# Performance work log

Hardware: AMD Instinct MI355X
Metric: run time of the kernel (lower is better)

## Reference

```python
import jax, jax.numpy as jnp
import numpy as np

B, S, D = 2, 2048, 1024
H, KS = 16, 64

def setup_inputs() -> dict:
    key = jax.random.key(0)
    k1, k2, k3, k4, k5 = jax.random.split(key, 5)
    return {
        "x": jax.random.normal(k1, (B, S, D), dtype=jnp.float32),
        "Wq": jax.random.normal(k2, (D, KS, H), dtype=jnp.float32) * 0.02,
        "Wk": jax.random.normal(k3, (D, KS, H), dtype=jnp.float32) * 0.02,
        "Wv": jax.random.normal(k4, (D, KS, H), dtype=jnp.float32) * 0.02,
        "kernel": jax.random.normal(k5, (H * KS, KS), dtype=jnp.float32) * 0.02,
    }

def reference(x, Wq, Wk, Wv, kernel):
    b, s, d = x.shape
    ks, h = Wq.shape[1], Wq.shape[2]
    # projections: heads-last layout [b, s, ks, h]
    q = jnp.einsum('bsd,dkh->bskh', x, Wq)
    k = jnp.einsum('bsd,dkh->bskh', x, Wk)
    v = jnp.einsum('bsd,dkh->bskh', x, Wv)
    # scores [b, i(query), l(key), h]
    scores = jnp.einsum('bikh,blkh->bilh', q, k) / jnp.sqrt(jnp.float32(ks))
    # strictly-upper-triangular (future) mask, as in the original:
    # band_part(ones,0,-1) - eye  ->  1 where l > i
    li = jnp.arange(s)
    mask = (li[None, :] > li[:, None]).astype(jnp.float32)  # [s, s]
    scores = scores - 1e8 * mask[None, :, :, None]
    weights = jax.nn.softmax(scores, axis=2)  # softmax over key axis l
    heads = jnp.einsum('bilh,blkh->bikh', weights, v)  # [b, s, ks, h]
    heads = heads.reshape(b, s, ks * h)  # row-major flatten of (ks, h), matching tf.reshape
    return heads @ kernel  # [b, s, ks]
```

## Files before the change

kernel.cpp:

```cpp
#include <hip/hip_runtime.h>
#include <hip/hip_bf16.h>

#define BB 2
#define SS 2048
#define DD 1024
#define HH 16
#define KSZ 64

typedef __attribute__((ext_vector_type(8))) short s16x8;
typedef __attribute__((ext_vector_type(4))) float f32x4;
typedef __attribute__((ext_vector_type(8))) unsigned short u16x8;
typedef __attribute__((ext_vector_type(4))) unsigned short u16x4;
typedef __attribute__((ext_vector_type(2))) unsigned int u32x2;
typedef unsigned short u16;

__device__ __forceinline__ u16 bf16rne(float f) {
  unsigned int u = __float_as_uint(f);
  unsigned int r = (u + 0x7FFFu + ((u >> 16) & 1u)) >> 16;
  return (u16)r;
}

__device__ __forceinline__ void lds_dma16(const u16* g, u16* l) {
  __builtin_amdgcn_global_load_lds(
      (const __attribute__((address_space(1))) unsigned int*)(const void*)g,
      (__attribute__((address_space(3))) unsigned int*)(void*)l, 16, 0, 0);
}

__global__ __launch_bounds__(256) void prep_all(
    const float* __restrict__ x, const float* __restrict__ Wq,
    const float* __restrict__ Wk, const float* __restrict__ Wv,
    const float* __restrict__ kern, u16* __restrict__ xb,
    u16* __restrict__ Wt, u16* __restrict__ BpT) {
  __shared__ float Ts[64][65];
  const int bid = blockIdx.x;
  const int tid = threadIdx.x;
  if (bid < 2048) {
    int idx = (bid * 256 + tid) * 8;
    float4 a = *(const float4*)(x + idx);
    float4 b = *(const float4*)(x + idx + 4);
    u16x8 v;
    v[0] = bf16rne(a.x); v[1] = bf16rne(a.y); v[2] = bf16rne(a.z); v[3] = bf16rne(a.w);
    v[4] = bf16rne(b.x); v[5] = bf16rne(b.y); v[6] = bf16rne(b.z); v[7] = bf16rne(b.w);
    *(u16x8*)(xb + idx) = v;
  } else if (bid < 2816) {
    const int bx = bid - 2048;
    const int p = bx >> 8, rem = bx & 255;
    const int d0 = (rem & 15) * 64, n0 = (rem >> 4) * 64;
    const float* W = (p == 0) ? Wq : (p == 1) ? Wk : Wv;
    u16* Wo = Wt + (size_t)p * DD * DD;
    #pragma unroll
    for (int i = 0; i < 4; ++i) {
      int f4 = tid + i * 256;
      int r = f4 >> 4, c4 = f4 & 15;
      float4 v = *(const float4*)(W + (size_t)(d0 + r) * DD + n0 + c4 * 4);
      Ts[r][c4 * 4 + 0] = v.x; Ts[r][c4 * 4 + 1] = v.y;
      Ts[r][c4 * 4 + 2] = v.z; Ts[r][c4 * 4 + 3] = v.w;
    }
    __syncthreads();
    #pragma unroll
    for (int i = 0; i < 4; ++i) {
      int ch = tid + i * 256;
      int n = ch >> 4, d4 = ch & 15;
      u16x4 o;
      #pragma unroll
      for (int j = 0; j < 4; ++j) o[j] = bf16rne(Ts[d4 * 4 + j][n]);
      *(u16x4*)(Wo + (size_t)(n0 + n) * DD + d0 + d4 * 4) = o;
    }
  } else {
    const int n = bid - 2816;
    const int k4 = tid * 4;
    u16x4 o;
    #pragma unroll
    for (int j = 0; j < 4; ++j) {
      int kp = k4 + j;
      int h = kp >> 6, k = kp & 63;
      o[j] = bf16rne(kern[(size_t)(k * HH + h) * KSZ + n]);
    }
    *(u16x4*)(BpT + (size_t)n * (HH * KSZ) + k4) = o;
  }
}

__global__ __launch_bounds__(256) void proj_kernel(
    const u16* __restrict__ xb, const u16* __restrict__ Wt,
    u16* __restrict__ qkvT) {
  const int xcd = blockIdx.x & 7;
  const int idx = blockIdx.x >> 3;
  const int mt = (xcd >> 1) * 8 + (idx & 7);
  const int nt = (xcd & 1) * 4 + ((idx >> 3) & 3);
  const int p  = idx >> 5;
  const int m0 = mt * 128, n0 = nt * 128;
  const u16* W = Wt + (size_t)p * DD * DD;
  u16* outp = qkvT + (size_t)p * (BB * HH * SS * KSZ);

  __shared__ __align__(16) unsigned char raw[34816];
  u16* As0 = (u16*)raw;
  u16* Bs0 = As0 + 128 * 32;
  u16* As1 = Bs0 + 128 * 32;
  u16* Bs1 = As1 + 128 * 32;
  u16* Cs  = (u16*)raw;

  const int tid = threadIdx.x;
  const int wave = tid >> 6, lane = tid & 63;
  const int g = lane >> 4, c = lane & 15;
  const int mbase = (wave & 1) * 64, nbase = (wave >> 1) * 64;

  const int lr = lane >> 2, lc = lane & 3;
  const int swz = (lc ^ ((lr >> 1) & 3)) * 8;
  const int rA0 = (wave * 2 + 0) * 16;
  const int rA1 = (wave * 2 + 1) * 16;
  const u16* srcA0 = xb + (size_t)(m0 + rA0 + lr) * DD + swz;
  const u16* srcA1 = xb + (size_t)(m0 + rA1 + lr) * DD + swz;
  const u16* srcB0 = W  + (size_t)(n0 + rA0 + lr) * DD + swz;
  const u16* srcB1 = W  + (size_t)(n0 + rA1 + lr) * DD + swz;
  const int sl0 = rA0 * 32, sl1 = rA1 * 32;

  f32x4 acc[4][4];
  #pragma unroll
  for (int i = 0; i < 4; ++i)
    #pragma unroll
    for (int j = 0; j < 4; ++j) acc[i][j] = {0.f, 0.f, 0.f, 0.f};

  lds_dma16(srcA0, As0 + sl0);  lds_dma16(srcA1, As0 + sl1);
  lds_dma16(srcB0, Bs0 + sl0);  lds_dma16(srcB1, Bs0 + sl1);
  __syncthreads();

  const int jsw = (c >> 1) & 3;
  #pragma unroll 2
  for (int t = 0; t < 32; ++t) {
    u16* Ac = (t & 1) ? As1 : As0;
    u16* Bc = (t & 1) ? Bs1 : Bs0;
    if (t < 31) {
      u16* An = (t & 1) ? As0 : As1;
      u16* Bn = (t & 1) ? Bs0 : Bs1;
      const int ko = (t + 1) * 32;
      lds_dma16(srcA0 + ko, An + sl0);  lds_dma16(srcA1 + ko, An + sl1);
      lds_dma16(srcB0 + ko, Bn + sl0);  lds_dma16(srcB1 + ko, Bn + sl1);
    }
    s16x8 af[4], bfr[4];
    #pragma unroll
    for (int mf = 0; mf < 4; ++mf)
      af[mf] = *(const s16x8*)&Ac[(mbase + mf * 16 + c) * 32 + ((g ^ jsw) * 8)];
    #pragma unroll
    for (int nf = 0; nf < 4; ++nf)
      bfr[nf] = *(const s16x8*)&Bc[(nbase + nf * 16 + c) * 32 + ((g ^ jsw) * 8)];
    #pragma unroll
    for (int mf = 0; mf < 4; ++mf)
      #pragma unroll
      for (int nf = 0; nf < 4; ++nf)
        acc[mf][nf] = __builtin_amdgcn_mfma_f32_16x16x32_bf16(
            af[mf], bfr[nf], acc[mf][nf], 0, 0, 0);
    __syncthreads();
  }

  const float cscale = (p == 0) ? 0.125f * 1.44269504f : 1.0f;
  #pragma unroll
  for (int mf = 0; mf < 4; ++mf)
    #pragma unroll
    for (int nf = 0; nf < 4; ++nf)
      #pragma unroll
      for (int r = 0; r < 4; ++r)
        Cs[(mbase + mf * 16 + g * 4 + r) * 136 + nbase + nf * 16 + c] =
            bf16rne(acc[mf][nf][r] * cscale);
  __syncthreads();
  const int b = m0 >> 11;
  if (p < 2) {
    int hh = tid >> 4, si = tid & 15;
    #pragma unroll
    for (int i = 0; i < 8; ++i) {
      int row = i * 16 + si;
      int s = (m0 + row) & 2047;
      u16x8 v;
      #pragma unroll
      for (int kp = 0; kp < 8; ++kp) v[kp] = Cs[row * 136 + kp * 16 + hh];
      *(u16x8*)(outp + ((size_t)(b * HH + hh) * SS + s) * KSZ + (n0 >> 4)) = v;
    }
  } else {
    const int s0 = m0 & 2047;
    #pragma unroll
    for (int i = 0; i < 8; ++i) {
      int chunk = tid + i * 256;
      int colid = chunk >> 4;
      int hh = colid >> 3, kp = colid & 7;
      int s8 = chunk & 15;
      u16x8 v;
      #pragma unroll
      for (int j = 0; j < 8; ++j) v[j] = Cs[(s8 * 8 + j) * 136 + kp * 16 + hh];
      *(u16x8*)(outp + ((size_t)(b * HH + hh) * KSZ + (n0 >> 4) + kp) * SS +
                s0 + s8 * 8) = v;
    }
  }
}

__global__ __launch_bounds__(256) void attn_kernel(
    const u16* __restrict__ qkvT, u16* __restrict__ headsB) {
  const int bid = blockIdx.x;
  const int hb = bid & 31;
  const int u  = bid >> 5;
  const int it = (u & 1) ? (31 - (u >> 1)) : (u >> 1);
  const int h = hb & 15, b = hb >> 4;
  const size_t plane = (size_t)(b * HH + h) * SS * KSZ;
  const size_t PSZ = (size_t)BB * HH * SS * KSZ;
  const u16* Qg = qkvT + plane;
  const u16* Kg = qkvT + PSZ + plane;
  const u16* Vg = qkvT + 2 * PSZ + plane;

  __shared__ u16 Ks[2][64 * 64];
  __shared__ u16 Vt[2][64 * 64];
  __shared__ u16 Ps[64 * 72];

  const int tid = threadIdx.x;
  const int lane = tid & 63;
  const int g = lane >> 4, c = lane & 15;
  const int wq0 = (tid >> 6) * 16;
  const int sr = tid >> 3, sc = tid & 7;
  const int soA = sr * 64 + ((sc ^ (sr & 7)) * 8);
  const int soB = soA + 32 * 64;

  s16x8 bq0 = *(const s16x8*)(Qg + (size_t)(it * 64 + wq0 + c) * KSZ + g * 8);
  s16x8 bq1 = *(const s16x8*)(Qg + (size_t)(it * 64 + wq0 + c) * KSZ + 32 + g * 8);

  u16x8 kr0 = *(const u16x8*)(Kg + (size_t)sr * KSZ + sc * 8);
  u16x8 kr1 = *(const u16x8*)(Kg + (size_t)(sr + 32) * KSZ + sc * 8);
  u16x8 vr0 = *(const u16x8*)(Vg + (size_t)sr * SS + sc * 8);
  u16x8 vr1 = *(const u16x8*)(Vg + (size_t)(sr + 32) * SS + sc * 8);
  *(u16x8*)&Ks[0][soA] = kr0; *(u16x8*)&Ks[0][soB] = kr1;
  *(u16x8*)&Vt[0][soA] = vr0; *(u16x8*)&Vt[0][soB] = vr1;
  if (it >= 1) {
    kr0 = *(const u16x8*)(Kg + (size_t)(64 + sr) * KSZ + sc * 8);
    kr1 = *(const u16x8*)(Kg + (size_t)(64 + sr + 32) * KSZ + sc * 8);
    vr0 = *(const u16x8*)(Vg + (size_t)sr * SS + 64 + sc * 8);
    vr1 = *(const u16x8*)(Vg + (size_t)(sr + 32) * SS + 64 + sc * 8);
  }
  __syncthreads();

  f32x4 o[4];
  #pragma unroll
  for (int mf = 0; mf < 4; ++mf) o[mf] = {0.f, 0.f, 0.f, 0.f};
  float l_i = 0.f;
  const int cswz = c & 7;

  #pragma unroll 1
  for (int t = 0; t <= it; ++t) {
    const int buf = t & 1;
    if (t < it) {
      const int nb = buf ^ 1;
      *(u16x8*)&Ks[nb][soA] = kr0; *(u16x8*)&Ks[nb][soB] = kr1;
      *(u16x8*)&Vt[nb][soA] = vr0; *(u16x8*)&Vt[nb][soB] = vr1;
      if (t + 2 <= it) {
        const int kv2 = t + 2;
        kr0 = *(const u16x8*)(Kg + (size_t)(kv2 * 64 + sr) * KSZ + sc * 8);
        kr1 = *(const u16x8*)(Kg + (size_t)(kv2 * 64 + sr + 32) * KSZ + sc * 8);
        vr0 = *(const u16x8*)(Vg + (size_t)sr * SS + kv2 * 64 + sc * 8);
        vr1 = *(const u16x8*)(Vg + (size_t)(sr + 32) * SS + kv2 * 64 + sc * 8);
      }
    }
    f32x4 s[4];
    #pragma unroll
    for (int mf = 0; mf < 4; ++mf) s[mf] = {0.f, 0.f, 0.f, 0.f};
    #pragma unroll
    for (int ks = 0; ks < 2; ++ks) {
      const s16x8 bq = ks ? bq1 : bq0;
      #pragma unroll
      for (int mf = 0; mf < 4; ++mf) {
        s16x8 ak = *(const s16x8*)&Ks[buf][(mf * 16 + c) * 64 +
                                          (((ks * 4 + g) ^ cswz) * 8)];
        s[mf] = __builtin_amdgcn_mfma_f32_16x16x32_bf16(ak, bq, s[mf], 0, 0, 0);
      }
    }
    if (t == it) {
      const int qloc = wq0 + c;
      #pragma unroll
      for (int mf = 0; mf < 4; ++mf)
        #pragma unroll
        for (int r = 0; r < 4; ++r)
          if (mf * 16 + g * 4 + r > qloc) s[mf][r] = -1e30f;
    }
    float ps = 0.f;
    #pragma unroll
    for (int mf = 0; mf < 4; ++mf) {
      float p0 = __builtin_amdgcn_exp2f(s[mf][0]);
      float p1 = __builtin_amdgcn_exp2f(s[mf][1]);
      float p2 = __builtin_amdgcn_exp2f(s[mf][2]);
      float p3 = __builtin_amdgcn_exp2f(s[mf][3]);
      ps += (p0 + p1) + (p2 + p3);
      u32x2 d;
      d[0] = (__float_as_uint(p0) >> 16) | (__float_as_uint(p1) & 0xFFFF0000u);
      d[1] = (__float_as_uint(p2) >> 16) | (__float_as_uint(p3) & 0xFFFF0000u);
      *(u32x2*)&Ps[(wq0 + c) * 72 + mf * 16 + g * 4] = d;
    }
    l_i += ps;
    #pragma unroll
    for (int ks = 0; ks < 2; ++ks) {
      s16x8 bp = *(const s16x8*)&Ps[(wq0 + c) * 72 + ks * 32 + g * 8];
      #pragma unroll
      for (int mf = 0; mf < 4; ++mf) {
        s16x8 av = *(const s16x8*)&Vt[buf][(mf * 16 + c) * 64 +
                                           (((ks * 4 + g) ^ cswz) * 8)];
        o[mf] = __builtin_amdgcn_mfma_f32_16x16x32_bf16(av, bp, o[mf], 0, 0, 0);
      }
    }
    __syncthreads();
  }
  l_i += __shfl_xor(l_i, 16);
  l_i += __shfl_xor(l_i, 32);
  const float inv = 1.0f / l_i;
  const int q = it * 64 + wq0 + c;
  #pragma unroll
  for (int mf = 0; mf < 4; ++mf) {
    u16x4 hv;
    #pragma unroll
    for (int r = 0; r < 4; ++r) hv[r] = bf16rne(o[mf][r] * inv);
    *(u16x4*)(headsB + plane + (size_t)q * KSZ + mf * 16 + g * 4) = hv;
  }
}

__global__ __launch_bounds__(256) void out_kernel(
    const u16* __restrict__ headsB, const u16* __restrict__ BpT,
    float* __restrict__ out) {
  const int m0 = blockIdx.x * 16;
  const int tid = threadIdx.x;
  const int wave = tid >> 6, lane = tid & 63;
  const int g = lane >> 4, c = lane & 15;

  const int m = m0 + c;
  const int b = m >> 11, s = m & 2047;

  f32x4 acc[4];
  #pragma unroll
  for (int nf = 0; nf < 4; ++nf) acc[nf] = {0.f, 0.f, 0.f, 0.f};

  #pragma unroll
  for (int it = 0; it < 8; ++it) {
    const int kb = wave * 256 + it * 32;
    const int hh = kb >> 6, kk = (kb & 63) + g * 8;
    s16x8 a = *(const s16x8*)(headsB +
        ((size_t)(b * HH + hh) * SS + s) * KSZ + kk);
    #pragma unroll
    for (int nf = 0; nf < 4; ++nf) {
      s16x8 bf = *(const s16x8*)(BpT +
          (size_t)(nf * 16 + c) * (HH * KSZ) + kb + g * 8);
      acc[nf] = __builtin_amdgcn_mfma_f32_16x16x32_bf16(a, bf, acc[nf], 0, 0, 0);
    }
  }

  __shared__ __align__(16) float red[4][64][16];
  #pragma unroll
  for (int nf = 0; nf < 4; ++nf)
    *(f32x4*)&red[wave][lane][nf * 4] = acc[nf];
  __syncthreads();

  const int mi = tid >> 4, n4 = (tid & 15) * 4;
  const int gg = mi >> 2, rr = mi & 3;
  float4 res;
  float* rp = &res.x;
  #pragma unroll
  for (int j = 0; j < 4; ++j) {
    int n = n4 + j;
    int cc = n & 15, nf = n >> 4;
    rp[j] = red[0][gg * 16 + cc][nf * 4 + rr] + red[1][gg * 16 + cc][nf * 4 + rr] +
            red[2][gg * 16 + cc][nf * 4 + rr] + red[3][gg * 16 + cc][nf * 4 + rr];
  }
  *(float4*)(out + (size_t)(m0 + mi) * KSZ + n4) = res;
}

extern "C" void kernel_launch(void* const* d_in, const int* in_sizes, int n_in,
                              void* d_out, int out_size, void* d_ws, size_t ws_size,
                              hipStream_t stream) {
  const float* x    = (const float*)d_in[0];
  const float* Wq   = (const float*)d_in[1];
  const float* Wk   = (const float*)d_in[2];
  const float* Wv   = (const float*)d_in[3];
  const float* kern = (const float*)d_in[4];
  float* out = (float*)d_out;

  u16* xb     = (u16*)d_ws;
  u16* Wt     = xb + (size_t)4096 * 1024;
  u16* qkvT   = Wt + (size_t)3 * 1024 * 1024;
  u16* headsB = qkvT + (size_t)3 * BB * HH * SS * KSZ;
  u16* BpT    = headsB + (size_t)BB * HH * SS * KSZ;

  prep_all<<<dim3(2880), 256, 0, stream>>>(x, Wq, Wk, Wv, kern, xb, Wt, BpT);
  proj_kernel<<<dim3(768), 256, 0, stream>>>(xb, Wt, qkvT);
  attn_kernel<<<dim3(1024), 256, 0, stream>>>(qkvT, headsB);
  out_kernel<<<dim3(256), 256, 0, stream>>>(headsB, BpT, out);
}
```

Baseline: 160.8 us.

## Halve projection M tile and load V fragments directly from global in attention

The projection GEMM moves from 128x128 to 64x128 tiles with twice as many blocks, a smaller LDS footprint and a launch bound of 6 waves-per-EU, aiming for better occupancy and CU fill. The attention kernel no longer stages V through shared memory. Each wave loads its V MFMA operands straight from global memory every KV step, which removes the LDS stores and reads for V. In exchange, the four waves now fetch the same V data redundantly, and those loads are not prefetched across iterations, so latency may be exposed.

```diff
diff --git a/kernel.cpp b/kernel.cpp
--- a/kernel.cpp
+++ b/kernel.cpp
@@ -80,48 +80,48 @@
   }
 }
 
-__global__ __launch_bounds__(256) void proj_kernel(
+__global__ __launch_bounds__(256, 6) void proj_kernel(
     const u16* __restrict__ xb, const u16* __restrict__ Wt,
     u16* __restrict__ qkvT) {
   const int xcd = blockIdx.x & 7;
   const int idx = blockIdx.x >> 3;
-  const int mt = (xcd >> 1) * 8 + (idx & 7);
-  const int nt = (xcd & 1) * 4 + ((idx >> 3) & 3);
-  const int p  = idx >> 5;
-  const int m0 = mt * 128, n0 = nt * 128;
+  const int mt = (xcd >> 1) * 16 + (idx & 15);
+  const int nt = (xcd & 1) * 4 + ((idx >> 4) & 3);
+  const int p  = idx >> 6;
+  const int m0 = mt * 64, n0 = nt * 128;
   const u16* W = Wt + (size_t)p * DD * DD;
   u16* outp = qkvT + (size_t)p * (BB * HH * SS * KSZ);
 
-  __shared__ __align__(16) unsigned char raw[34816];
+  __shared__ __align__(16) unsigned char raw[24576];
   u16* As0 = (u16*)raw;
-  u16* Bs0 = As0 + 128 * 32;
+  u16* Bs0 = As0 + 64 * 32;
   u16* As1 = Bs0 + 128 * 32;
-  u16* Bs1 = As1 + 128 * 32;
+  u16* Bs1 = As1 + 64 * 32;
   u16* Cs  = (u16*)raw;
 
   const int tid = threadIdx.x;
   const int wave = tid >> 6, lane = tid & 63;
   const int g = lane >> 4, c = lane & 15;
-  const int mbase = (wave & 1) * 64, nbase = (wave >> 1) * 64;
+  const int mbase = (wave & 1) * 32, nbase = (wave >> 1) * 64;
 
   const int lr = lane >> 2, lc = lane & 3;
   const int swz = (lc ^ ((lr >> 1) & 3)) * 8;
-  const int rA0 = (wave * 2 + 0) * 16;
-  const int rA1 = (wave * 2 + 1) * 16;
-  const u16* srcA0 = xb + (size_t)(m0 + rA0 + lr) * DD + swz;
-  const u16* srcA1 = xb + (size_t)(m0 + rA1 + lr) * DD + swz;
-  const u16* srcB0 = W  + (size_t)(n0 + rA0 + lr) * DD + swz;
-  const u16* srcB1 = W  + (size_t)(n0 + rA1 + lr) * DD + swz;
-  const int sl0 = rA0 * 32, sl1 = rA1 * 32;
-
-  f32x4 acc[4][4];
-  #pragma unroll
-  for (int i = 0; i < 4; ++i)
+  const int rA  = wave * 16;
+  const int rB0 = (wave * 2 + 0) * 16;
+  const int rB1 = (wave * 2 + 1) * 16;
+  const u16* srcA  = xb + (size_t)(m0 + rA  + lr) * DD + swz;
+  const u16* srcB0 = W  + (size_t)(n0 + rB0 + lr) * DD + swz;
+  const u16* srcB1 = W  + (size_t)(n0 + rB1 + lr) * DD + swz;
+  const int slA = rA * 32, slB0 = rB0 * 32, slB1 = rB1 * 32;
+
+  f32x4 acc[2][4];
+  #pragma unroll
+  for (int i = 0; i < 2; ++i)
     #pragma unroll
     for (int j = 0; j < 4; ++j) acc[i][j] = {0.f, 0.f, 0.f, 0.f};
 
-  lds_dma16(srcA0, As0 + sl0);  lds_dma16(srcA1, As0 + sl1);
-  lds_dma16(srcB0, Bs0 + sl0);  lds_dma16(srcB1, Bs0 + sl1);
+  lds_dma16(srcA, As0 + slA);
+  lds_dma16(srcB0, Bs0 + slB0);  lds_dma16(srcB1, Bs0 + slB1);
   __syncthreads();
 
   const int jsw = (c >> 1) & 3;
@@ -133,18 +133,18 @@
       u16* An = (t & 1) ? As0 : As1;
       u16* Bn = (t & 1) ? Bs0 : Bs1;
       const int ko = (t + 1) * 32;
-      lds_dma16(srcA0 + ko, An + sl0);  lds_dma16(srcA1 + ko, An + sl1);
-      lds_dma16(srcB0 + ko, Bn + sl0);  lds_dma16(srcB1 + ko, Bn + sl1);
-    }
-    s16x8 af[4], bfr[4];
-    #pragma unroll
-    for (int mf = 0; mf < 4; ++mf)
+      lds_dma16(srcA + ko, An + slA);
+      lds_dma16(srcB0 + ko, Bn + slB0);  lds_dma16(srcB1 + ko, Bn + slB1);
+    }
+    s16x8 af[2], bfr[4];
+    #pragma unroll
+    for (int mf = 0; mf < 2; ++mf)
       af[mf] = *(const s16x8*)&Ac[(mbase + mf * 16 + c) * 32 + ((g ^ jsw) * 8)];
     #pragma unroll
     for (int nf = 0; nf < 4; ++nf)
       bfr[nf] = *(const s16x8*)&Bc[(nbase + nf * 16 + c) * 32 + ((g ^ jsw) * 8)];
     #pragma unroll
-    for (int mf = 0; mf < 4; ++mf)
+    for (int mf = 0; mf < 2; ++mf)
       #pragma unroll
       for (int nf = 0; nf < 4; ++nf)
         acc[mf][nf] = __builtin_amdgcn_mfma_f32_16x16x32_bf16(
@@ -154,7 +154,7 @@
 
   const float cscale = (p == 0) ? 0.125f * 1.44269504f : 1.0f;
   #pragma unroll
-  for (int mf = 0; mf < 4; ++mf)
+  for (int mf = 0; mf < 2; ++mf)
     #pragma unroll
     for (int nf = 0; nf < 4; ++nf)
       #pragma unroll
@@ -166,7 +166,7 @@
   if (p < 2) {
     int hh = tid >> 4, si = tid & 15;
     #pragma unroll
-    for (int i = 0; i < 8; ++i) {
+    for (int i = 0; i < 4; ++i) {
       int row = i * 16 + si;
       int s = (m0 + row) & 2047;
       u16x8 v;
@@ -177,11 +177,11 @@
   } else {
     const int s0 = m0 & 2047;
     #pragma unroll
-    for (int i = 0; i < 8; ++i) {
+    for (int i = 0; i < 4; ++i) {
       int chunk = tid + i * 256;
-      int colid = chunk >> 4;
+      int colid = chunk >> 3;
       int hh = colid >> 3, kp = colid & 7;
-      int s8 = chunk & 15;
+      int s8 = chunk & 7;
       u16x8 v;
       #pragma unroll
       for (int j = 0; j < 8; ++j) v[j] = Cs[(s8 * 8 + j) * 136 + kp * 16 + hh];
@@ -205,7 +205,6 @@
   const u16* Vg = qkvT + 2 * PSZ + plane;
 
   __shared__ u16 Ks[2][64 * 64];
-  __shared__ u16 Vt[2][64 * 64];
   __shared__ u16 Ps[64 * 72];
 
   const int tid = threadIdx.x;
@@ -219,17 +218,14 @@
   s16x8 bq0 = *(const s16x8*)(Qg + (size_t)(it * 64 + wq0 + c) * KSZ + g * 8);
   s16x8 bq1 = *(const s16x8*)(Qg + (size_t)(it * 64 + wq0 + c) * KSZ + 32 + g * 8);
 
+  const u16* vb = Vg + (size_t)c * SS + g * 8;
+
   u16x8 kr0 = *(const u16x8*)(Kg + (size_t)sr * KSZ + sc * 8);
   u16x8 kr1 = *(const u16x8*)(Kg + (size_t)(sr + 32) * KSZ + sc * 8);
-  u16x8 vr0 = *(const u16x8*)(Vg + (size_t)sr * SS + sc * 8);
-  u16x8 vr1 = *(const u16x8*)(Vg + (size_t)(sr + 32) * SS + sc * 8);
   *(u16x8*)&Ks[0][soA] = kr0; *(u16x8*)&Ks[0][soB] = kr1;
-  *(u16x8*)&Vt[0][soA] = vr0; *(u16x8*)&Vt[0][soB] = vr1;
   if (it >= 1) {
     kr0 = *(const u16x8*)(Kg + (size_t)(64 + sr) * KSZ + sc * 8);
     kr1 = *(const u16x8*)(Kg + (size_t)(64 + sr + 32) * KSZ + sc * 8);
-    vr0 = *(const u16x8*)(Vg + (size_t)sr * SS + 64 + sc * 8);
-    vr1 = *(const u16x8*)(Vg + (size_t)(sr + 32) * SS + 64 + sc * 8);
   }
   __syncthreads();
 
@@ -245,15 +241,19 @@
     if (t < it) {
       const int nb = buf ^ 1;
       *(u16x8*)&Ks[nb][soA] = kr0; *(u16x8*)&Ks[nb][soB] = kr1;
-      *(u16x8*)&Vt[nb][soA] = vr0; *(u16x8*)&Vt[nb][soB] = vr1;
       if (t + 2 <= it) {
         const int kv2 = t + 2;
         kr0 = *(const u16x8*)(Kg + (size_t)(kv2 * 64 + sr) * KSZ + sc * 8);
         kr1 = *(const u16x8*)(Kg + (size_t)(kv2 * 64 + sr + 32) * KSZ + sc * 8);
-        vr0 = *(const u16x8*)(Vg + (size_t)sr * SS + kv2 * 64 + sc * 8);
-        vr1 = *(const u16x8*)(Vg + (size_t)(sr + 32) * SS + kv2 * 64 + sc * 8);
       }
     }
+    s16x8 av[2][4];
+    #pragma unroll
+    for (int ks = 0; ks < 2; ++ks)
+      #pragma unroll
+      for (int mf = 0; mf < 4; ++mf)
+        av[ks][mf] = *(const s16x8*)(vb + (size_t)(mf * 16) * SS +
+                                     t * 64 + ks * 32);
     f32x4 s[4];
     #pragma unroll
     for (int mf = 0; mf < 4; ++mf) s[mf] = {0.f, 0.f, 0.f, 0.f};
@@ -293,11 +293,9 @@
     for (int ks = 0; ks < 2; ++ks) {
       s16x8 bp = *(const s16x8*)&Ps[(wq0 + c) * 72 + ks * 32 + g * 8];
       #pragma unroll
-      for (int mf = 0; mf < 4; ++mf) {
-        s16x8 av = *(const s16x8*)&Vt[buf][(mf * 16 + c) * 64 +
-                                           (((ks * 4 + g) ^ cswz) * 8)];
-        o[mf] = __builtin_amdgcn_mfma_f32_16x16x32_bf16(av, bp, o[mf], 0, 0, 0);
-      }
+      for (int mf = 0; mf < 4; ++mf)
+        o[mf] = __builtin_amdgcn_mfma_f32_16x16x32_bf16(av[ks][mf], bp, o[mf],
+                                                        0, 0, 0);
     }
     __syncthreads();
   }
@@ -380,7 +378,7 @@
   u16* BpT    = headsB + (size_t)BB * HH * SS * KSZ;
 
   prep_all<<<dim3(2880), 256, 0, stream>>>(x, Wq, Wk, Wv, kern, xb, Wt, BpT);
-  proj_kernel<<<dim3(768), 256, 0, stream>>>(xb, Wt, qkvT);
+  proj_kernel<<<dim3(1536), 256, 0, stream>>>(xb, Wt, qkvT);
   attn_kernel<<<dim3(1024), 256, 0, stream>>>(qkvT, headsB);
   out_kernel<<<dim3(256), 256, 0, stream>>>(headsB, BpT, out);
 }
```

Measured after the change: 232.9 us. +44.8%, slower.
